# Performance work log

Measured on AMD Instinct MI355X. Metric: run time of the kernel, lower is better.

Reference implementation:

```python
import jax, jax.numpy as jnp
import numpy as np

N = 50000
IN_DIM, HID, OUT = 128, 64, 128
HEADS = 4
EPS_LN = 1e-5
NEG_SLOPE = 0.2


def gat_conv(x, W, a_src, a_dst, bias, src, dst, concat):
    """PyG-style GATConv. x:[N,F], W:[F,H*C], a_src/a_dst:[H,C], src/dst:[E]."""
    H, C = a_src.shape
    h = (x @ W).reshape(-1, H, C)                 # [N,H,C]
    e_src = jnp.sum(h * a_src, axis=-1)           # [N,H]
    e_dst = jnp.sum(h * a_dst, axis=-1)           # [N,H]
    e = jax.nn.leaky_relu(e_src[src] + e_dst[dst], NEG_SLOPE)  # [E,H]
    # softmax over incoming edges per destination node (numerically stable)
    m = jax.ops.segment_max(e, dst, num_segments=N)            # [N,H]
    m = jnp.where(jnp.isfinite(m), m, 0.0)
    ex = jnp.exp(e - m[dst])                                   # [E,H]
    denom = jax.ops.segment_sum(ex, dst, num_segments=N)       # [N,H]
    alpha = ex / (denom[dst] + 1e-16)                          # [E,H]
    msg = h[src] * alpha[:, :, None]                           # [E,H,C]
    out = jax.ops.segment_sum(msg, dst, num_segments=N)        # [N,H,C]
    out = out.reshape(-1, H * C) if concat else out.mean(axis=1)
    return out + bias


def layer_norm(x, gamma, beta):
    mu = jnp.mean(x, axis=-1, keepdims=True)
    var = jnp.mean(jnp.square(x - mu), axis=-1, keepdims=True)
    return (x - mu) * jax.lax.rsqrt(var + EPS_LN) * gamma + beta


def setup_inputs() -> dict:
    key = jax.random.key(0)
    ks = jax.random.split(key, 12)
    x = jax.random.normal(ks[0], (N, IN_DIM), dtype=jnp.float32)
    edge_index = jax.random.randint(ks[1], (2, 800000), 0, N, dtype=jnp.int64)
    s1 = 1.0 / np.sqrt(IN_DIM)
    W1 = jax.random.normal(ks[2], (IN_DIM, HEADS * HID), dtype=jnp.float32) * s1
    a_src1 = jax.random.normal(ks[3], (HEADS, HID), dtype=jnp.float32) * 0.1
    a_dst1 = jax.random.normal(ks[4], (HEADS, HID), dtype=jnp.float32) * 0.1
    b1 = jnp.zeros((HEADS * HID,), dtype=jnp.float32)
    s2 = 1.0 / np.sqrt(HEADS * HID)
    W2 = jax.random.normal(ks[5], (HEADS * HID, HEADS * OUT), dtype=jnp.float32) * s2
    a_src2 = jax.random.normal(ks[6], (HEADS, OUT), dtype=jnp.float32) * 0.1
    a_dst2 = jax.random.normal(ks[7], (HEADS, OUT), dtype=jnp.float32) * 0.1
    b2 = jnp.zeros((OUT,), dtype=jnp.float32)
    gamma = jnp.ones((OUT,), dtype=jnp.float32)
    beta = jnp.zeros((OUT,), dtype=jnp.float32)
    return {"x": x, "edge_index": edge_index, "W1": W1, "a_src1": a_src1,
            "a_dst1": a_dst1, "b1": b1, "W2": W2, "a_src2": a_src2,
            "a_dst2": a_dst2, "b2": b2, "gamma": gamma, "beta": beta}


def reference(x, edge_index, W1, a_src1, a_dst1, b1, W2, a_src2, a_dst2, b2, gamma, beta):
    # PyG GATConv adds self loops by default
    loop = jnp.arange(N, dtype=edge_index.dtype)
    src = jnp.concatenate([edge_index[0], loop])
    dst = jnp.concatenate([edge_index[1], loop])
    h = gat_conv(x, W1, a_src1, a_dst1, b1, src, dst, concat=True)   # [N, 256]
    h = jax.nn.relu(h)
    h = gat_conv(h, W2, a_src2, a_dst2, b2, src, dst, concat=False)  # [N, 128]
    return layer_norm(h, gamma, beta)
```

## Files before the change

kernel.cpp:

```cpp
#include <hip/hip_runtime.h>
#include <hip/hip_fp16.h>
#include <cstdint>
#include <cstddef>


constexpr int NNODES = 50000;
constexpr int NBINS = (NNODES + 255) >> 8;
constexpr int ABLOCKS = 256;

typedef unsigned short bf16_t;
typedef __attribute__((ext_vector_type(8))) short bf16x8;
typedef __attribute__((ext_vector_type(4))) float f32x4;

__device__ __forceinline__ float bf2f(bf16_t b) {
  return __uint_as_float(((unsigned int)b) << 16);
}
__device__ __forceinline__ bf16_t f2bf(float f) {
  unsigned int u = __float_as_uint(f);
  u += 0x7fffu + ((u >> 16) & 1u);
  return (bf16_t)(u >> 16);
}
__device__ __forceinline__ float4 bf4_to_f4(ushort4 v) {
  return make_float4(bf2f(v.x), bf2f(v.y), bf2f(v.z), bf2f(v.w));
}
__device__ __forceinline__ ushort4 f4_to_bf4(float4 v) {
  return make_ushort4(f2bf(v.x), f2bf(v.y), f2bf(v.z), f2bf(v.w));
}
__device__ __forceinline__ ushort f2h(float f) {
  __half h = __float2half_rn(f);
  return *(ushort*)&h;
}
__device__ __forceinline__ float h2f(ushort u) {
  __half h; *(ushort*)&h = u;
  return __half2float(h);
}
__device__ __forceinline__ float lrelu(float x) { return x > 0.f ? x : 0.2f * x; }
__device__ __forceinline__ int clampi(int v, int lo, int hi) {
  return v < lo ? lo : (v > hi ? hi : v);
}
__device__ __forceinline__ int load_edge(const void* ei, int mode, int idx) {
  if (mode) return (int)((const long long*)ei)[idx];
  return ((const int*)ei)[idx];
}


__global__ void convert_x_kernel(const float* __restrict__ x, bf16_t* __restrict__ xb,
                                 int n4) {
  int i = blockIdx.x * blockDim.x + threadIdx.x;
  if (i >= n4) return;
  float4 v = *(const float4*)(x + 4 * (size_t)i);
  *(ushort4*)(xb + 4 * (size_t)i) = f4_to_bf4(v);
}

template <int K, int NC>
__global__ void transpose_w_kernel(const float* __restrict__ W, bf16_t* __restrict__ Wt) {
  int n = blockIdx.x;
  int k = threadIdx.x;
  Wt[(size_t)n * K + k] = f2bf(W[(size_t)k * NC + n]);
}

__global__ void proj2_kernel(const float* __restrict__ W2,
                             const float* __restrict__ asrc2,
                             const float* __restrict__ adst2,
                             float* __restrict__ ws2, float* __restrict__ wd2) {
  int h = blockIdx.x;
  int k = threadIdx.x;
  const float* wrow = W2 + (size_t)k * 512 + h * 128;
  const float* as = asrc2 + h * 128;
  const float* ad = adst2 + h * 128;
  float s = 0.f, d = 0.f;
  for (int c = 0; c < 128; ++c) { s += wrow[c] * as[c]; d += wrow[c] * ad[c]; }
  ws2[h * 256 + k] = s;
  wd2[h * 256 + k] = d;
}

__global__ __launch_bounds__(1024) void wstack_kernel(const float* __restrict__ W2,
                                                      bf16_t* __restrict__ Wt2s) {
  int c = blockIdx.x;
  int t = threadIdx.x;
  int h = t >> 8, k = t & 255;
  Wt2s[(size_t)c * 1024 + t] = f2bf(W2[(size_t)k * 512 + h * 128 + c] * 0.25f);
}

__global__ void detect_kernel(const int* __restrict__ ei32, int* __restrict__ mode) {
  __shared__ int nz;
  if (threadIdx.x == 0) nz = 0;
  __syncthreads();
  int idx = 2 * threadIdx.x + 1;
  if (ei32[idx] != 0) atomicAdd(&nz, 1);
  __syncthreads();
  if (threadIdx.x == 0) mode[0] = (nz == 0) ? 1 : 0;
}

__global__ __launch_bounds__(256) void binhist_kernel(
    const void* __restrict__ ei, const int* __restrict__ modep,
    int* __restrict__ blockBin, int e0, int et, int chunk) {
  __shared__ int h[NBINS];
  int t = threadIdx.x, blk = blockIdx.x;
  for (int i = t; i < NBINS; i += 256) h[i] = 0;
  __syncthreads();
  int mode = modep[0];
  int lo = blk * chunk, hi = min(et, lo + chunk);
  for (int e = lo + t; e < hi; e += 256) {
    int dst = (e < e0) ? load_edge(ei, mode, e0 + e) : (e - e0);
    dst = clampi(dst, 0, NNODES - 1);
    atomicAdd(&h[dst >> 8], 1);
  }
  __syncthreads();
  for (int i = t; i < NBINS; i += 256) blockBin[i * ABLOCKS + blk] = h[i];
}

__global__ __launch_bounds__(ABLOCKS) void binscanA_kernel(int* __restrict__ blockBin,
                                                           int* __restrict__ binTotal) {
  __shared__ int sm[ABLOCKS];
  int b = blockIdx.x, t = threadIdx.x;
  int orig = blockBin[b * ABLOCKS + t];
  sm[t] = orig;
  __syncthreads();
  for (int off = 1; off < ABLOCKS; off <<= 1) {
    int u = (t >= off) ? sm[t - off] : 0;
    __syncthreads();
    sm[t] += u;
    __syncthreads();
  }
  blockBin[b * ABLOCKS + t] = sm[t] - orig;
  if (t == ABLOCKS - 1) binTotal[b] = sm[ABLOCKS - 1];
}

__global__ __launch_bounds__(256) void binscanB_kernel(const int* __restrict__ binTotal,
                                                       int* __restrict__ binStart) {
  __shared__ int sm[256];
  int t = threadIdx.x;
  int orig = (t < NBINS) ? binTotal[t] : 0;
  sm[t] = orig;
  __syncthreads();
  for (int off = 1; off < 256; off <<= 1) {
    int u = (t >= off) ? sm[t - off] : 0;
    __syncthreads();
    sm[t] += u;
    __syncthreads();
  }
  if (t < NBINS) binStart[t] = sm[t] - orig;
  if (t == 255) binStart[NBINS] = sm[255];
}

__global__ __launch_bounds__(256) void binscatter_kernel(
    const void* __restrict__ ei, const int* __restrict__ modep,
    const int* __restrict__ blockBin, const int* __restrict__ binStart,
    int2* __restrict__ pairs, int e0, int et, int chunk) {
  __shared__ int cur[NBINS];
  int t = threadIdx.x, blk = blockIdx.x;
  for (int i = t; i < NBINS; i += 256)
    cur[i] = binStart[i] + blockBin[i * ABLOCKS + blk];
  __syncthreads();
  int mode = modep[0];
  int lo = blk * chunk, hi = min(et, lo + chunk);
  for (int e = lo + t; e < hi; e += 256) {
    int src, dst;
    if (e < e0) { src = load_edge(ei, mode, e); dst = load_edge(ei, mode, e0 + e); }
    else        { src = dst = e - e0; }
    src = clampi(src, 0, NNODES - 1);
    dst = clampi(dst, 0, NNODES - 1);
    int p = atomicAdd(&cur[dst >> 8], 1);
    pairs[p] = make_int2(src, dst);
  }
}

__global__ __launch_bounds__(256) void csrbin_kernel(const int2* __restrict__ pairs,
                                                     const int* __restrict__ binStart,
                                                     int* __restrict__ rowptr,
                                                     int* __restrict__ col) {
  __shared__ int cnt[256];
  __shared__ int sc[256];
  int b = blockIdx.x, t = threadIdx.x;
  int node0 = b << 8;
  int es = binStart[b], ee = binStart[b + 1];
  cnt[t] = 0;
  __syncthreads();
  for (int p = es + t; p < ee; p += 256) {
    int2 pr = pairs[p];
    int d = clampi(pr.y - node0, 0, 255);
    atomicAdd(&cnt[d], 1);
  }
  __syncthreads();
  int orig = cnt[t];
  sc[t] = orig;
  __syncthreads();
  for (int off = 1; off < 256; off <<= 1) {
    int u = (t >= off) ? sc[t - off] : 0;
    __syncthreads();
    sc[t] += u;
    __syncthreads();
  }
  int excl = sc[t] - orig;
  if (node0 + t < NNODES) rowptr[node0 + t] = es + excl;
  if (b == NBINS - 1 && t == 0) rowptr[NNODES] = ee;
  cnt[t] = excl;
  __syncthreads();
  for (int p = es + t; p < ee; p += 256) {
    int2 pr = pairs[p];
    int d = clampi(pr.y - node0, 0, 255);
    int pos = atomicAdd(&cnt[d], 1);
    col[es + pos] = pr.x;
  }
}

__global__ __launch_bounds__(256) void gemm1s_kernel(
    const bf16_t* __restrict__ A, const bf16_t* __restrict__ Wt,
    bf16_t* __restrict__ C, const float* __restrict__ asrc,
    const float* __restrict__ adst, float* __restrict__ es,
    float* __restrict__ ed, int M) {
  __shared__ __align__(16) ushort As[64 * 40];
  __shared__ __align__(16) ushort Bs[64 * 40];
  const int t    = threadIdx.x;
  const int wv   = t >> 6;
  const int lane = t & 63;
  const int m    = lane & 15;
  const int quad = lane >> 4;
  const int bm = blockIdx.x * 64, bn = blockIdx.y * 64;
  const int srow = t & 63;
  const int sk8  = t >> 6;

  f32x4 acc0 = {0.f, 0.f, 0.f, 0.f};
  f32x4 acc1 = {0.f, 0.f, 0.f, 0.f};
  f32x4 acc2 = {0.f, 0.f, 0.f, 0.f};
  f32x4 acc3 = {0.f, 0.f, 0.f, 0.f};

  for (int k0 = 0; k0 < 128; k0 += 32) {
    int ga = clampi(bm + srow, 0, M - 1);
    float4 av = *(const float4*)(A + (size_t)ga * 128 + k0 + sk8 * 8);
    *(float4*)(&As[srow * 40 + sk8 * 8]) = av;
    float4 bv = *(const float4*)(Wt + (size_t)(bn + srow) * 128 + k0 + sk8 * 8);
    *(float4*)(&Bs[srow * 40 + sk8 * 8]) = bv;
    __syncthreads();

    bf16x8 af = *(const bf16x8*)(&As[(wv * 16 + m) * 40 + quad * 8]);
    bf16x8 b0 = *(const bf16x8*)(&Bs[(0 * 16 + m) * 40 + quad * 8]);
    bf16x8 b1 = *(const bf16x8*)(&Bs[(1 * 16 + m) * 40 + quad * 8]);
    bf16x8 b2 = *(const bf16x8*)(&Bs[(2 * 16 + m) * 40 + quad * 8]);
    bf16x8 b3 = *(const bf16x8*)(&Bs[(3 * 16 + m) * 40 + quad * 8]);
    acc0 = __builtin_amdgcn_mfma_f32_16x16x32_bf16(af, b0, acc0, 0, 0, 0);
    acc1 = __builtin_amdgcn_mfma_f32_16x16x32_bf16(af, b1, acc1, 0, 0, 0);
    acc2 = __builtin_amdgcn_mfma_f32_16x16x32_bf16(af, b2, acc2, 0, 0, 0);
    acc3 = __builtin_amdgcn_mfma_f32_16x16x32_bf16(af, b3, acc3, 0, 0, 0);
    __syncthreads();
  }

  float as0 = asrc[bn +  0 + m], as1 = asrc[bn + 16 + m];
  float as2 = asrc[bn + 32 + m], as3 = asrc[bn + 48 + m];
  float ad0 = adst[bn +  0 + m], ad1 = adst[bn + 16 + m];
  float ad2 = adst[bn + 32 + m], ad3 = adst[bn + 48 + m];
  const int hd = bn >> 6;

#pragma unroll
  for (int r = 0; r < 4; ++r) {
    int row = bm + wv * 16 + quad * 4 + r;
    float ps = acc0[r] * as0 + acc1[r] * as1 + acc2[r] * as2 + acc3[r] * as3;
    float pd = acc0[r] * ad0 + acc1[r] * ad1 + acc2[r] * ad2 + acc3[r] * ad3;
    for (int mm = 1; mm < 16; mm <<= 1) {
      ps += __shfl_xor(ps, mm);
      pd += __shfl_xor(pd, mm);
    }
    if (row < M) {
      size_t base = (size_t)row * 256 + bn;
      C[base +  0 + m] = f2bf(acc0[r]);
      C[base + 16 + m] = f2bf(acc1[r]);
      C[base + 32 + m] = f2bf(acc2[r]);
      C[base + 48 + m] = f2bf(acc3[r]);
      if (m == 0) {
        es[row * 4 + hd] = ps;
        ed[row * 4 + hd] = pd;
      }
    }
  }
}

__global__ __launch_bounds__(256) void alpha_kernel(
    const float* __restrict__ es, const float* __restrict__ ed,
    const int* __restrict__ rowptr, const int* __restrict__ col,
    ushort* __restrict__ alpha) {
  int node = (blockIdx.x * blockDim.x + threadIdx.x) >> 6;
  if (node >= NNODES) return;
  int lane = threadIdx.x & 63;
  int beg = rowptr[node], end = rowptr[node + 1];
  float4 edv = *(const float4*)(ed + node * 4);
  float4 l = make_float4(0.f, 0.f, 0.f, 0.f);
  for (int p = beg + lane; p < end; p += 64) {
    int s = col[p];
    float4 e = *(const float4*)(es + s * 4);
    l.x += __expf(lrelu(e.x + edv.x));
    l.y += __expf(lrelu(e.y + edv.y));
    l.z += __expf(lrelu(e.z + edv.z));
    l.w += __expf(lrelu(e.w + edv.w));
  }
  for (int off = 1; off < 64; off <<= 1) {
    l.x += __shfl_xor(l.x, off);
    l.y += __shfl_xor(l.y, off);
    l.z += __shfl_xor(l.z, off);
    l.w += __shfl_xor(l.w, off);
  }
  float4 il = make_float4(1.f / (l.x + 1e-16f), 1.f / (l.y + 1e-16f),
                          1.f / (l.z + 1e-16f), 1.f / (l.w + 1e-16f));
  for (int p = beg + lane; p < end; p += 64) {
    int s = col[p];
    float4 e = *(const float4*)(es + s * 4);
    ushort4 a;
    a.x = f2h(__expf(lrelu(e.x + edv.x)) * il.x);
    a.y = f2h(__expf(lrelu(e.y + edv.y)) * il.y);
    a.z = f2h(__expf(lrelu(e.z + edv.z)) * il.z);
    a.w = f2h(__expf(lrelu(e.w + edv.w)) * il.w);
    *(ushort4*)(alpha + (size_t)p * 4) = a;
  }
}

__global__ __launch_bounds__(256) void aggregate1_kernel(
    const bf16_t* __restrict__ h, const ushort* __restrict__ alpha,
    const int* __restrict__ rowptr, const int* __restrict__ col,
    const float* __restrict__ b1, bf16_t* __restrict__ out,
    const float* __restrict__ ws2, const float* __restrict__ wd2,
    float* __restrict__ es2, float* __restrict__ ed2) {
  int node = (blockIdx.x * blockDim.x + threadIdx.x) >> 6;
  if (node >= NNODES) return;
  int lane = threadIdx.x & 63;
  int head = lane >> 4;
  int beg = rowptr[node], end = rowptr[node + 1];
  const ushort4* hb = (const ushort4*)h;
  float4 acc = make_float4(0.f, 0.f, 0.f, 0.f);
  int j = beg;
  for (; j + 4 <= end; j += 4) {
    int s0 = col[j], s1 = col[j + 1], s2 = col[j + 2], s3 = col[j + 3];
    ushort u0 = alpha[(size_t)(j + 0) * 4 + head];
    ushort u1 = alpha[(size_t)(j + 1) * 4 + head];
    ushort u2 = alpha[(size_t)(j + 2) * 4 + head];
    ushort u3 = alpha[(size_t)(j + 3) * 4 + head];
    ushort4 r0 = hb[(size_t)s0 * 64 + lane];
    ushort4 r1 = hb[(size_t)s1 * 64 + lane];
    ushort4 r2 = hb[(size_t)s2 * 64 + lane];
    ushort4 r3 = hb[(size_t)s3 * 64 + lane];
    float a0 = h2f(u0), a1 = h2f(u1), a2 = h2f(u2), a3 = h2f(u3);
    float4 v0 = bf4_to_f4(r0), v1 = bf4_to_f4(r1);
    float4 v2 = bf4_to_f4(r2), v3 = bf4_to_f4(r3);
    acc.x += a0 * v0.x + a1 * v1.x + a2 * v2.x + a3 * v3.x;
    acc.y += a0 * v0.y + a1 * v1.y + a2 * v2.y + a3 * v3.y;
    acc.z += a0 * v0.z + a1 * v1.z + a2 * v2.z + a3 * v3.z;
    acc.w += a0 * v0.w + a1 * v1.w + a2 * v2.w + a3 * v3.w;
  }
  for (; j < end; ++j) {
    int s0 = col[j];
    float a0 = h2f(alpha[(size_t)j * 4 + head]);
    float4 v0 = bf4_to_f4(hb[(size_t)s0 * 64 + lane]);
    acc.x += a0 * v0.x;
    acc.y += a0 * v0.y;
    acc.z += a0 * v0.z;
    acc.w += a0 * v0.w;
  }
  float4 bb = *(const float4*)(b1 + 4 * lane);
  float4 o;
  o.x = fmaxf(acc.x + bb.x, 0.f);
  o.y = fmaxf(acc.y + bb.y, 0.f);
  o.z = fmaxf(acc.z + bb.z, 0.f);
  o.w = fmaxf(acc.w + bb.w, 0.f);
  *(ushort4*)(out + (size_t)node * 256 + 4 * lane) = f4_to_bf4(o);

  float s2[4], d2[4];
#pragma unroll
  for (int hh = 0; hh < 4; ++hh) {
    float4 wv = *(const float4*)(ws2 + hh * 256 + 4 * lane);
    float4 dv = *(const float4*)(wd2 + hh * 256 + 4 * lane);
    s2[hh] = o.x * wv.x + o.y * wv.y + o.z * wv.z + o.w * wv.w;
    d2[hh] = o.x * dv.x + o.y * dv.y + o.z * dv.z + o.w * dv.w;
  }
  for (int mm = 1; mm < 64; mm <<= 1) {
#pragma unroll
    for (int hh = 0; hh < 4; ++hh) {
      s2[hh] += __shfl_xor(s2[hh], mm);
      d2[hh] += __shfl_xor(d2[hh], mm);
    }
  }
  if (lane == 0) {
#pragma unroll
    for (int hh = 0; hh < 4; ++hh) {
      es2[node * 4 + hh] = s2[hh];
      ed2[node * 4 + hh] = d2[hh];
    }
  }
}

__device__ __forceinline__ void fma4h(float (&acc)[4][4], ushort4 q, float4 v) {
  float f0 = h2f(q.x), f1 = h2f(q.y), f2 = h2f(q.z), f3 = h2f(q.w);
  acc[0][0] += f0 * v.x; acc[0][1] += f0 * v.y; acc[0][2] += f0 * v.z; acc[0][3] += f0 * v.w;
  acc[1][0] += f1 * v.x; acc[1][1] += f1 * v.y; acc[1][2] += f1 * v.z; acc[1][3] += f1 * v.w;
  acc[2][0] += f2 * v.x; acc[2][1] += f2 * v.y; acc[2][2] += f2 * v.z; acc[2][3] += f2 * v.w;
  acc[3][0] += f3 * v.x; acc[3][1] += f3 * v.y; acc[3][2] += f3 * v.z; acc[3][3] += f3 * v.w;
}

__global__ __launch_bounds__(256) void agg2in_kernel(
    const bf16_t* __restrict__ out1, const ushort* __restrict__ alpha,
    const int* __restrict__ rowptr, const int* __restrict__ col,
    bf16_t* __restrict__ z, int n0, int n1) {
  int node = n0 + ((blockIdx.x * blockDim.x + threadIdx.x) >> 6);
  if (node >= n1) return;
  int lane = threadIdx.x & 63;
  int beg = rowptr[node], end = rowptr[node + 1];
  const ushort4* hb = (const ushort4*)out1;
  float acc[4][4] = {{0.f,0.f,0.f,0.f},{0.f,0.f,0.f,0.f},
                     {0.f,0.f,0.f,0.f},{0.f,0.f,0.f,0.f}};
  int j = beg;
  for (; j + 4 <= end; j += 4) {
    int s0 = col[j], s1 = col[j + 1], s2 = col[j + 2], s3 = col[j + 3];
    ushort4 q0 = *(const ushort4*)(alpha + (size_t)(j + 0) * 4);
    ushort4 q1 = *(const ushort4*)(alpha + (size_t)(j + 1) * 4);
    ushort4 q2 = *(const ushort4*)(alpha + (size_t)(j + 2) * 4);
    ushort4 q3 = *(const ushort4*)(alpha + (size_t)(j + 3) * 4);
    ushort4 r0 = hb[(size_t)s0 * 64 + lane];
    ushort4 r1 = hb[(size_t)s1 * 64 + lane];
    ushort4 r2 = hb[(size_t)s2 * 64 + lane];
    ushort4 r3 = hb[(size_t)s3 * 64 + lane];
    fma4h(acc, q0, bf4_to_f4(r0));
    fma4h(acc, q1, bf4_to_f4(r1));
    fma4h(acc, q2, bf4_to_f4(r2));
    fma4h(acc, q3, bf4_to_f4(r3));
  }
  for (; j < end; ++j) {
    int s0 = col[j];
    ushort4 q0 = *(const ushort4*)(alpha + (size_t)j * 4);
    ushort4 r0 = hb[(size_t)s0 * 64 + lane];
    fma4h(acc, q0, bf4_to_f4(r0));
  }
  bf16_t* zr = z + (size_t)(node - n0) * 1024 + 4 * lane;
#pragma unroll
  for (int h = 0; h < 4; ++h) {
    *(ushort4*)(zr + h * 256) =
        f4_to_bf4(make_float4(acc[h][0], acc[h][1], acc[h][2], acc[h][3]));
  }
}

__global__ __launch_bounds__(256) void gemm2ln_kernel(
    const bf16_t* __restrict__ Z, const bf16_t* __restrict__ Wt2s,
    const float* __restrict__ b2, const float* __restrict__ gamma,
    const float* __restrict__ beta, float* __restrict__ out, int n0, int M) {
  __shared__ __align__(16) ushort As[64 * 40];
  __shared__ __align__(16) ushort Bs[128 * 40];
  const int t    = threadIdx.x;
  const int wv   = t >> 6;
  const int lane = t & 63;
  const int m    = lane & 15;
  const int quad = lane >> 4;
  const int bm   = blockIdx.x * 64;

  f32x4 c0 = {0.f,0.f,0.f,0.f}, c1 = c0, c2 = c0, c3 = c0;
  f32x4 c4 = c0, c5 = c0, c6 = c0, c7 = c0;

  const int arow = t & 63, ak8 = t >> 6;
  for (int k0 = 0; k0 < 1024; k0 += 32) {
    int ga = clampi(bm + arow, 0, M - 1);
    *(float4*)(&As[arow * 40 + ak8 * 8]) =
        *(const float4*)(Z + (size_t)ga * 1024 + k0 + ak8 * 8);
    {
      int q = t;
      *(float4*)(&Bs[(q >> 2) * 40 + (q & 3) * 8]) =
          *(const float4*)(Wt2s + (size_t)(q >> 2) * 1024 + k0 + (q & 3) * 8);
      q = t + 256;
      *(float4*)(&Bs[(q >> 2) * 40 + (q & 3) * 8]) =
          *(const float4*)(Wt2s + (size_t)(q >> 2) * 1024 + k0 + (q & 3) * 8);
    }
    __syncthreads();

    bf16x8 af = *(const bf16x8*)(&As[(wv * 16 + m) * 40 + quad * 8]);
    bf16x8 b0 = *(const bf16x8*)(&Bs[(0 * 16 + m) * 40 + quad * 8]);
    bf16x8 b1 = *(const bf16x8*)(&Bs[(1 * 16 + m) * 40 + quad * 8]);
    bf16x8 b2f = *(const bf16x8*)(&Bs[(2 * 16 + m) * 40 + quad * 8]);
    bf16x8 b3 = *(const bf16x8*)(&Bs[(3 * 16 + m) * 40 + quad * 8]);
    bf16x8 b4 = *(const bf16x8*)(&Bs[(4 * 16 + m) * 40 + quad * 8]);
    bf16x8 b5 = *(const bf16x8*)(&Bs[(5 * 16 + m) * 40 + quad * 8]);
    bf16x8 b6 = *(const bf16x8*)(&Bs[(6 * 16 + m) * 40 + quad * 8]);
    bf16x8 b7 = *(const bf16x8*)(&Bs[(7 * 16 + m) * 40 + quad * 8]);
    c0 = __builtin_amdgcn_mfma_f32_16x16x32_bf16(af, b0, c0, 0, 0, 0);
    c1 = __builtin_amdgcn_mfma_f32_16x16x32_bf16(af, b1, c1, 0, 0, 0);
    c2 = __builtin_amdgcn_mfma_f32_16x16x32_bf16(af, b2f, c2, 0, 0, 0);
    c3 = __builtin_amdgcn_mfma_f32_16x16x32_bf16(af, b3, c3, 0, 0, 0);
    c4 = __builtin_amdgcn_mfma_f32_16x16x32_bf16(af, b4, c4, 0, 0, 0);
    c5 = __builtin_amdgcn_mfma_f32_16x16x32_bf16(af, b5, c5, 0, 0, 0);
    c6 = __builtin_amdgcn_mfma_f32_16x16x32_bf16(af, b6, c6, 0, 0, 0);
    c7 = __builtin_amdgcn_mfma_f32_16x16x32_bf16(af, b7, c7, 0, 0, 0);
    __syncthreads();
  }

  float b2v[8], gv[8], btv[8];
#pragma unroll
  for (int n = 0; n < 8; ++n) {
    int c = n * 16 + m;
    b2v[n] = b2[c]; gv[n] = gamma[c]; btv[n] = beta[c];
  }
#pragma unroll
  for (int r = 0; r < 4; ++r) {
    float v0 = c0[r] + b2v[0], v1 = c1[r] + b2v[1];
    float v2 = c2[r] + b2v[2], v3 = c3[r] + b2v[3];
    float v4 = c4[r] + b2v[4], v5 = c5[r] + b2v[5];
    float v6 = c6[r] + b2v[6], v7 = c7[r] + b2v[7];
    float tsum = v0 + v1 + v2 + v3 + v4 + v5 + v6 + v7;
    tsum += __shfl_xor(tsum, 1); tsum += __shfl_xor(tsum, 2);
    tsum += __shfl_xor(tsum, 4); tsum += __shfl_xor(tsum, 8);
    float mu = tsum * (1.f / 128.f);
    float d0 = v0 - mu, d1 = v1 - mu, d2 = v2 - mu, d3 = v3 - mu;
    float d4 = v4 - mu, d5 = v5 - mu, d6 = v6 - mu, d7 = v7 - mu;
    float vq = d0*d0 + d1*d1 + d2*d2 + d3*d3 + d4*d4 + d5*d5 + d6*d6 + d7*d7;
    vq += __shfl_xor(vq, 1); vq += __shfl_xor(vq, 2);
    vq += __shfl_xor(vq, 4); vq += __shfl_xor(vq, 8);
    float rinv = rsqrtf(vq * (1.f / 128.f) + 1e-5f);
    int row = bm + wv * 16 + quad * 4 + r;
    if (row < M) {
      float* orow = out + (size_t)(n0 + row) * 128;
      orow[0 * 16 + m] = d0 * rinv * gv[0] + btv[0];
      orow[1 * 16 + m] = d1 * rinv * gv[1] + btv[1];
      orow[2 * 16 + m] = d2 * rinv * gv[2] + btv[2];
      orow[3 * 16 + m] = d3 * rinv * gv[3] + btv[3];
      orow[4 * 16 + m] = d4 * rinv * gv[4] + btv[4];
      orow[5 * 16 + m] = d5 * rinv * gv[5] + btv[5];
      orow[6 * 16 + m] = d6 * rinv * gv[6] + btv[6];
      orow[7 * 16 + m] = d7 * rinv * gv[7] + btv[7];
    }
  }
}


extern "C" void kernel_launch(void* const* d_in, const int* in_sizes, int n_in,
                              void* d_out, int out_size, void* d_ws, size_t ws_size,
                              hipStream_t stream) {
  const float* x     = (const float*)d_in[0];
  const void*  ei    = d_in[1];
  const float* W1    = (const float*)d_in[2];
  const float* asrc1 = (const float*)d_in[3];
  const float* adst1 = (const float*)d_in[4];
  const float* b1    = (const float*)d_in[5];
  const float* W2    = (const float*)d_in[6];
  const float* asrc2 = (const float*)d_in[7];
  const float* adst2 = (const float*)d_in[8];
  const float* b2    = (const float*)d_in[9];
  const float* gamma = (const float*)d_in[10];
  const float* beta  = (const float*)d_in[11];
  float* out = (float*)d_out;

  const int E0 = in_sizes[1] / 2;
  const int ET = E0 + NNODES;

  char* w = (char*)d_ws;
  bf16_t* z      = (bf16_t*)(w + 0);
  int2*   pairs  = (int2*)(w + 25600000);
  bf16_t* h1     = (bf16_t*)(w + 25600000);
  bf16_t* xb     = (bf16_t*)(w + 51200000);
  bf16_t* out1   = (bf16_t*)(w + 51200000);
  ushort* alpha  = (ushort*)(w + 76800000);
  float* es    = (float*)(w + 83600000);
  float* ed    = (float*)(w + 84400000);
  bf16_t* Wt1    = (bf16_t*)(w + 85200000);
  bf16_t* Wt2s   = (bf16_t*)(w + 85300000);
  float* ws2   = (float*)(w + 85564000);
  float* wd2   = (float*)(w + 85570000);
  int* rowptr   = (int*)(w + 85600000);
  int* binStart = (int*)(w + 85800064);
  int* binTotal = (int*)(w + 85801000);
  int* blockBin = (int*)(w + 85802000);
  int* col      = (int*)(w + 86200192);
  int* mode     = (int*)(w + 89600704);

  convert_x_kernel<<<(NNODES * 128 / 4 + 255) / 256, 256, 0, stream>>>(x, xb,
                                                                       NNODES * 128 / 4);
  transpose_w_kernel<128, 256><<<256, 128, 0, stream>>>(W1, Wt1);
  proj2_kernel<<<4, 256, 0, stream>>>(W2, asrc2, adst2, ws2, wd2);
  wstack_kernel<<<128, 1024, 0, stream>>>(W2, Wt2s);

  const int CHUNK = (ET + ABLOCKS - 1) / ABLOCKS;
  detect_kernel<<<1, 256, 0, stream>>>((const int*)ei, mode);
  binhist_kernel<<<ABLOCKS, 256, 0, stream>>>(ei, mode, blockBin, E0, ET, CHUNK);
  binscanA_kernel<<<NBINS, ABLOCKS, 0, stream>>>(blockBin, binTotal);
  binscanB_kernel<<<1, 256, 0, stream>>>(binTotal, binStart);
  binscatter_kernel<<<ABLOCKS, 256, 0, stream>>>(ei, mode, blockBin, binStart, pairs,
                                                 E0, ET, CHUNK);
  csrbin_kernel<<<NBINS, 256, 0, stream>>>(pairs, binStart, rowptr, col);

  const int MB = (NNODES + 63) / 64;
  const int NODE_BLOCKS = (NNODES + 3) / 4;

  gemm1s_kernel<<<dim3(MB, 4), 256, 0, stream>>>(xb, Wt1, h1, asrc1, adst1,
                                                 es, ed, NNODES);
  alpha_kernel<<<NODE_BLOCKS, 256, 0, stream>>>(es, ed, rowptr, col, alpha);
  aggregate1_kernel<<<NODE_BLOCKS, 256, 0, stream>>>(h1, alpha, rowptr, col, b1,
                                                     out1, ws2, wd2, es, ed);

  alpha_kernel<<<NODE_BLOCKS, 256, 0, stream>>>(es, ed, rowptr, col, alpha);

  const int HALF = NNODES / 2;
  const int AB = (HALF * 64 + 255) / 256;
  const int GB = (HALF + 63) / 64;
  agg2in_kernel<<<AB, 256, 0, stream>>>(out1, alpha, rowptr, col, z, 0, HALF);
  gemm2ln_kernel<<<GB, 256, 0, stream>>>(z, Wt2s, b2, gamma, beta, out, 0, HALF);
  agg2in_kernel<<<AB, 256, 0, stream>>>(out1, alpha, rowptr, col, z, HALF, NNODES);
  gemm2ln_kernel<<<GB, 256, 0, stream>>>(z, Wt2s, b2, gamma, beta, out, HALF, HALF);
}
```

Baseline: 407.6 us.

## Use 16-lane groups for alpha and split-wave edge processing in aggregation

The alpha kernel now assigns 16 lanes per node instead of a full 64-lane wavefront, which suits the average degree of about 17. The two aggregation kernels split each wavefront into two halves that handle alternate edges with 16-byte bf16x8 gathers per lane. The halves are combined with a cross-half shuffle, which roughly halves the serial edge-loop length per node and widens each memory access. In exchange it adds shuffle reductions, drops the 4-edge unrolling, and increases register use for the layer-2 accumulators (32 floats per lane).

```diff
diff --git a/kernel.cpp b/kernel.cpp
--- a/kernel.cpp
+++ b/kernel.cpp
@@ -279,13 +279,13 @@
     const float* __restrict__ es, const float* __restrict__ ed,
     const int* __restrict__ rowptr, const int* __restrict__ col,
     ushort* __restrict__ alpha) {
-  int node = (blockIdx.x * blockDim.x + threadIdx.x) >> 6;
+  int node = (blockIdx.x * blockDim.x + threadIdx.x) >> 4;
   if (node >= NNODES) return;
-  int lane = threadIdx.x & 63;
+  int l16 = threadIdx.x & 15;
   int beg = rowptr[node], end = rowptr[node + 1];
   float4 edv = *(const float4*)(ed + node * 4);
   float4 l = make_float4(0.f, 0.f, 0.f, 0.f);
-  for (int p = beg + lane; p < end; p += 64) {
+  for (int p = beg + l16; p < end; p += 16) {
     int s = col[p];
     float4 e = *(const float4*)(es + s * 4);
     l.x += __expf(lrelu(e.x + edv.x));
@@ -293,7 +293,7 @@
     l.z += __expf(lrelu(e.z + edv.z));
     l.w += __expf(lrelu(e.w + edv.w));
   }
-  for (int off = 1; off < 64; off <<= 1) {
+  for (int off = 1; off < 16; off <<= 1) {
     l.x += __shfl_xor(l.x, off);
     l.y += __shfl_xor(l.y, off);
     l.z += __shfl_xor(l.z, off);
@@ -301,7 +301,7 @@
   }
   float4 il = make_float4(1.f / (l.x + 1e-16f), 1.f / (l.y + 1e-16f),
                           1.f / (l.z + 1e-16f), 1.f / (l.w + 1e-16f));
-  for (int p = beg + lane; p < end; p += 64) {
+  for (int p = beg + l16; p < end; p += 16) {
     int s = col[p];
     float4 e = *(const float4*)(es + s * 4);
     ushort4 a;
@@ -322,55 +322,57 @@
   int node = (blockIdx.x * blockDim.x + threadIdx.x) >> 6;
   if (node >= NNODES) return;
   int lane = threadIdx.x & 63;
-  int head = lane >> 4;
+  int half = lane >> 5;
+  int cl   = lane & 31;
+  int head = cl >> 3;
   int beg = rowptr[node], end = rowptr[node + 1];
-  const ushort4* hb = (const ushort4*)h;
-  float4 acc = make_float4(0.f, 0.f, 0.f, 0.f);
+  float acc[8] = {0.f, 0.f, 0.f, 0.f, 0.f, 0.f, 0.f, 0.f};
   int j = beg;
-  for (; j + 4 <= end; j += 4) {
-    int s0 = col[j], s1 = col[j + 1], s2 = col[j + 2], s3 = col[j + 3];
-    ushort u0 = alpha[(size_t)(j + 0) * 4 + head];
-    ushort u1 = alpha[(size_t)(j + 1) * 4 + head];
-    ushort u2 = alpha[(size_t)(j + 2) * 4 + head];
-    ushort u3 = alpha[(size_t)(j + 3) * 4 + head];
-    ushort4 r0 = hb[(size_t)s0 * 64 + lane];
-    ushort4 r1 = hb[(size_t)s1 * 64 + lane];
-    ushort4 r2 = hb[(size_t)s2 * 64 + lane];
-    ushort4 r3 = hb[(size_t)s3 * 64 + lane];
-    float a0 = h2f(u0), a1 = h2f(u1), a2 = h2f(u2), a3 = h2f(u3);
-    float4 v0 = bf4_to_f4(r0), v1 = bf4_to_f4(r1);
-    float4 v2 = bf4_to_f4(r2), v3 = bf4_to_f4(r3);
-    acc.x += a0 * v0.x + a1 * v1.x + a2 * v2.x + a3 * v3.x;
-    acc.y += a0 * v0.y + a1 * v1.y + a2 * v2.y + a3 * v3.y;
-    acc.z += a0 * v0.z + a1 * v1.z + a2 * v2.z + a3 * v3.z;
-    acc.w += a0 * v0.w + a1 * v1.w + a2 * v2.w + a3 * v3.w;
-  }
-  for (; j < end; ++j) {
-    int s0 = col[j];
-    float a0 = h2f(alpha[(size_t)j * 4 + head]);
-    float4 v0 = bf4_to_f4(hb[(size_t)s0 * 64 + lane]);
-    acc.x += a0 * v0.x;
-    acc.y += a0 * v0.y;
-    acc.z += a0 * v0.z;
-    acc.w += a0 * v0.w;
-  }
-  float4 bb = *(const float4*)(b1 + 4 * lane);
-  float4 o;
-  o.x = fmaxf(acc.x + bb.x, 0.f);
-  o.y = fmaxf(acc.y + bb.y, 0.f);
-  o.z = fmaxf(acc.z + bb.z, 0.f);
-  o.w = fmaxf(acc.w + bb.w, 0.f);
-  *(ushort4*)(out + (size_t)node * 256 + 4 * lane) = f4_to_bf4(o);
+  for (; j + 2 <= end; j += 2) {
+    int e = j + half;
+    int s = col[e];
+    float a = h2f(alpha[(size_t)e * 4 + head]);
+    bf16x8 r = *(const bf16x8*)(h + (size_t)s * 256 + 8 * cl);
+#pragma unroll
+    for (int i = 0; i < 8; ++i) acc[i] += a * bf2f((ushort)r[i]);
+  }
+  if (j < end && half == 0) {
+    int s = col[j];
+    float a = h2f(alpha[(size_t)j * 4 + head]);
+    bf16x8 r = *(const bf16x8*)(h + (size_t)s * 256 + 8 * cl);
+#pragma unroll
+    for (int i = 0; i < 8; ++i) acc[i] += a * bf2f((ushort)r[i]);
+  }
+#pragma unroll
+  for (int i = 0; i < 8; ++i) acc[i] += __shfl_xor(acc[i], 32);
+
+  float4 bA = *(const float4*)(b1 + 8 * cl);
+  float4 bB = *(const float4*)(b1 + 8 * cl + 4);
+  float o[8];
+  o[0] = fmaxf(acc[0] + bA.x, 0.f);  o[1] = fmaxf(acc[1] + bA.y, 0.f);
+  o[2] = fmaxf(acc[2] + bA.z, 0.f);  o[3] = fmaxf(acc[3] + bA.w, 0.f);
+  o[4] = fmaxf(acc[4] + bB.x, 0.f);  o[5] = fmaxf(acc[5] + bB.y, 0.f);
+  o[6] = fmaxf(acc[6] + bB.z, 0.f);  o[7] = fmaxf(acc[7] + bB.w, 0.f);
+  if (half == 0) {
+    bf16x8 ov;
+#pragma unroll
+    for (int i = 0; i < 8; ++i) ov[i] = (short)f2bf(o[i]);
+    *(bf16x8*)(out + (size_t)node * 256 + 8 * cl) = ov;
+  }
 
   float s2[4], d2[4];
 #pragma unroll
   for (int hh = 0; hh < 4; ++hh) {
-    float4 wv = *(const float4*)(ws2 + hh * 256 + 4 * lane);
-    float4 dv = *(const float4*)(wd2 + hh * 256 + 4 * lane);
-    s2[hh] = o.x * wv.x + o.y * wv.y + o.z * wv.z + o.w * wv.w;
-    d2[hh] = o.x * dv.x + o.y * dv.y + o.z * dv.z + o.w * dv.w;
-  }
-  for (int mm = 1; mm < 64; mm <<= 1) {
+    float4 wA = *(const float4*)(ws2 + hh * 256 + 8 * cl);
+    float4 wB = *(const float4*)(ws2 + hh * 256 + 8 * cl + 4);
+    float4 dA = *(const float4*)(wd2 + hh * 256 + 8 * cl);
+    float4 dB = *(const float4*)(wd2 + hh * 256 + 8 * cl + 4);
+    s2[hh] = o[0]*wA.x + o[1]*wA.y + o[2]*wA.z + o[3]*wA.w +
+             o[4]*wB.x + o[5]*wB.y + o[6]*wB.z + o[7]*wB.w;
+    d2[hh] = o[0]*dA.x + o[1]*dA.y + o[2]*dA.z + o[3]*dA.w +
+             o[4]*dB.x + o[5]*dB.y + o[6]*dB.z + o[7]*dB.w;
+  }
+  for (int mm = 1; mm < 32; mm <<= 1) {
 #pragma unroll
     for (int hh = 0; hh < 4; ++hh) {
       s2[hh] += __shfl_xor(s2[hh], mm);
@@ -384,14 +386,6 @@
       ed2[node * 4 + hh] = d2[hh];
     }
   }
-}
-
-__device__ __forceinline__ void fma4h(float (&acc)[4][4], ushort4 q, float4 v) {
-  float f0 = h2f(q.x), f1 = h2f(q.y), f2 = h2f(q.z), f3 = h2f(q.w);
-  acc[0][0] += f0 * v.x; acc[0][1] += f0 * v.y; acc[0][2] += f0 * v.z; acc[0][3] += f0 * v.w;
-  acc[1][0] += f1 * v.x; acc[1][1] += f1 * v.y; acc[1][2] += f1 * v.z; acc[1][3] += f1 * v.w;
-  acc[2][0] += f2 * v.x; acc[2][1] += f2 * v.y; acc[2][2] += f2 * v.z; acc[2][3] += f2 * v.w;
-  acc[3][0] += f3 * v.x; acc[3][1] += f3 * v.y; acc[3][2] += f3 * v.z; acc[3][3] += f3 * v.w;
 }
 
 __global__ __launch_bounds__(256) void agg2in_kernel(
@@ -401,37 +395,61 @@
   int node = n0 + ((blockIdx.x * blockDim.x + threadIdx.x) >> 6);
   if (node >= n1) return;
   int lane = threadIdx.x & 63;
+  int half = lane >> 5;
+  int cl   = lane & 31;
   int beg = rowptr[node], end = rowptr[node + 1];
-  const ushort4* hb = (const ushort4*)out1;
-  float acc[4][4] = {{0.f,0.f,0.f,0.f},{0.f,0.f,0.f,0.f},
-                     {0.f,0.f,0.f,0.f},{0.f,0.f,0.f,0.f}};
+  float acc[4][8] = {{0.f,0.f,0.f,0.f,0.f,0.f,0.f,0.f},
+                     {0.f,0.f,0.f,0.f,0.f,0.f,0.f,0.f},
+                     {0.f,0.f,0.f,0.f,0.f,0.f,0.f,0.f},
+                     {0.f,0.f,0.f,0.f,0.f,0.f,0.f,0.f}};
   int j = beg;
-  for (; j + 4 <= end; j += 4) {
-    int s0 = col[j], s1 = col[j + 1], s2 = col[j + 2], s3 = col[j + 3];
-    ushort4 q0 = *(const ushort4*)(alpha + (size_t)(j + 0) * 4);
-    ushort4 q1 = *(const ushort4*)(alpha + (size_t)(j + 1) * 4);
-    ushort4 q2 = *(const ushort4*)(alpha + (size_t)(j + 2) * 4);
-    ushort4 q3 = *(const ushort4*)(alpha + (size_t)(j + 3) * 4);
-    ushort4 r0 = hb[(size_t)s0 * 64 + lane];
-    ushort4 r1 = hb[(size_t)s1 * 64 + lane];
-    ushort4 r2 = hb[(size_t)s2 * 64 + lane];
-    ushort4 r3 = hb[(size_t)s3 * 64 + lane];
-    fma4h(acc, q0, bf4_to_f4(r0));
-    fma4h(acc, q1, bf4_to_f4(r1));
-    fma4h(acc, q2, bf4_to_f4(r2));
-    fma4h(acc, q3, bf4_to_f4(r3));
-  }
-  for (; j < end; ++j) {
-    int s0 = col[j];
-    ushort4 q0 = *(const ushort4*)(alpha + (size_t)j * 4);
-    ushort4 r0 = hb[(size_t)s0 * 64 + lane];
-    fma4h(acc, q0, bf4_to_f4(r0));
-  }
-  bf16_t* zr = z + (size_t)(node - n0) * 1024 + 4 * lane;
-#pragma unroll
-  for (int h = 0; h < 4; ++h) {
-    *(ushort4*)(zr + h * 256) =
-        f4_to_bf4(make_float4(acc[h][0], acc[h][1], acc[h][2], acc[h][3]));
+  for (; j + 2 <= end; j += 2) {
+    int e = j + half;
+    int s = col[e];
+    ushort4 q = *(const ushort4*)(alpha + (size_t)e * 4);
+    bf16x8 r = *(const bf16x8*)(out1 + (size_t)s * 256 + 8 * cl);
+    float a0 = h2f(q.x), a1 = h2f(q.y), a2 = h2f(q.z), a3 = h2f(q.w);
+    float v[8];
+#pragma unroll
+    for (int i = 0; i < 8; ++i) v[i] = bf2f((ushort)r[i]);
+#pragma unroll
+    for (int i = 0; i < 8; ++i) {
+      acc[0][i] += a0 * v[i];
+      acc[1][i] += a1 * v[i];
+      acc[2][i] += a2 * v[i];
+      acc[3][i] += a3 * v[i];
+    }
+  }
+  if (j < end && half == 0) {
+    int s = col[j];
+    ushort4 q = *(const ushort4*)(alpha + (size_t)j * 4);
+    bf16x8 r = *(const bf16x8*)(out1 + (size_t)s * 256 + 8 * cl);
+    float a0 = h2f(q.x), a1 = h2f(q.y), a2 = h2f(q.z), a3 = h2f(q.w);
+    float v[8];
+#pragma unroll
+    for (int i = 0; i < 8; ++i) v[i] = bf2f((ushort)r[i]);
+#pragma unroll
+    for (int i = 0; i < 8; ++i) {
+      acc[0][i] += a0 * v[i];
+      acc[1][i] += a1 * v[i];
+      acc[2][i] += a2 * v[i];
+      acc[3][i] += a3 * v[i];
+    }
+  }
+#pragma unroll
+  for (int hh = 0; hh < 4; ++hh)
+#pragma unroll
+    for (int i = 0; i < 8; ++i) acc[hh][i] += __shfl_xor(acc[hh][i], 32);
+
+  if (half == 0) {
+    bf16_t* zr = z + (size_t)(node - n0) * 1024 + 8 * cl;
+#pragma unroll
+    for (int hh = 0; hh < 4; ++hh) {
+      bf16x8 ov;
+#pragma unroll
+      for (int i = 0; i < 8; ++i) ov[i] = (short)f2bf(acc[hh][i]);
+      *(bf16x8*)(zr + hh * 256) = ov;
+    }
   }
 }
 
@@ -581,14 +599,15 @@
 
   const int MB = (NNODES + 63) / 64;
   const int NODE_BLOCKS = (NNODES + 3) / 4;
+  const int NODE_BLOCKS16 = (NNODES * 16 + 255) / 256;
 
   gemm1s_kernel<<<dim3(MB, 4), 256, 0, stream>>>(xb, Wt1, h1, asrc1, adst1,
                                                  es, ed, NNODES);
-  alpha_kernel<<<NODE_BLOCKS, 256, 0, stream>>>(es, ed, rowptr, col, alpha);
+  alpha_kernel<<<NODE_BLOCKS16, 256, 0, stream>>>(es, ed, rowptr, col, alpha);
   aggregate1_kernel<<<NODE_BLOCKS, 256, 0, stream>>>(h1, alpha, rowptr, col, b1,
                                                      out1, ws2, wd2, es, ed);
 
-  alpha_kernel<<<NODE_BLOCKS, 256, 0, stream>>>(es, ed, rowptr, col, alpha);
+  alpha_kernel<<<NODE_BLOCKS16, 256, 0, stream>>>(es, ed, rowptr, col, alpha);
 
   const int HALF = NNODES / 2;
   const int AB = (HALF * 64 + 255) / 256;
```

Result: slower. 435.2 us (+6.8%).
